# Kernel tuning notes

Hardware: AMD Instinct MI355X
Metric: run time of the kernel (lower is better)

Reference implementation:

```python
import jax, jax.numpy as jnp
import numpy as np

TOPK = 1024
C = 32
FC0 = 256
EPS_BN = 1e-5
EPS_NORM = 1e-12


def setup_inputs() -> dict:
    key = jax.random.key(0)
    ks = jax.random.split(key, 8)
    B, L = 128, 16384
    N = B * L
    x = jax.random.normal(ks[0], (N, C), dtype=jnp.float32)
    length = jnp.full((B,), L, dtype=jnp.int32)
    # conv1d_1: Conv1d(32, 1, 1) -> weight [1, 32, 1] ~ vector [32], bias [1]
    w_att = jax.random.normal(ks[1], (C,), dtype=jnp.float32) * (1.0 / np.sqrt(C))
    b_att = jnp.zeros((1,), dtype=jnp.float32)
    # bn_1: BatchNorm1d(1) (eval mode: use running stats)
    g1 = jnp.ones((1,), dtype=jnp.float32)
    be1 = jnp.zeros((1,), dtype=jnp.float32)
    rm1 = jnp.zeros((1,), dtype=jnp.float32)
    rv1 = jnp.ones((1,), dtype=jnp.float32)
    # fc_1: Linear(TOPK*C, FC0)
    fan_in = TOPK * C
    W_fc = jax.random.normal(ks[2], (FC0, fan_in), dtype=jnp.float32) * (1.0 / np.sqrt(fan_in))
    b_fc = jnp.zeros((FC0,), dtype=jnp.float32)
    # bn_2: BatchNorm1d(FC0) (eval mode)
    g2 = jnp.ones((FC0,), dtype=jnp.float32)
    be2 = jnp.zeros((FC0,), dtype=jnp.float32)
    rm2 = jnp.zeros((FC0,), dtype=jnp.float32)
    rv2 = jnp.ones((FC0,), dtype=jnp.float32)
    return {"x": x, "length": length, "w_att": w_att, "b_att": b_att,
            "g1": g1, "be1": be1, "rm1": rm1, "rv1": rv1,
            "W_fc": W_fc, "b_fc": b_fc,
            "g2": g2, "be2": be2, "rm2": rm2, "rv2": rv2}


def reference(x, length, w_att, b_att, g1, be1, rm1, rv1, W_fc, b_fc, g2, be2, rm2, rv2):
    B = length.shape[0]
    N = x.shape[0]
    L = N // B  # equal-length segments (sum(length) == N)
    # attention score: 1x1 conv over channels + BatchNorm1d(1) (eval)
    att = x @ w_att + b_att[0]                                   # [N]
    att = (att - rm1[0]) * (g1[0] / jnp.sqrt(rv1[0] + EPS_BN)) + be1[0]
    # per-segment descending sort + take top TOPK == top_k per segment
    att_b = att.reshape(B, L)                                    # [B, L]
    x_b = x.reshape(B, L, C)                                     # [B, L, C]
    _, idx = jax.lax.top_k(att_b, TOPK)                          # [B, TOPK]
    ranked = jnp.take_along_axis(x_b, idx[:, :, None], axis=1)   # [B, TOPK, C]
    flat = ranked.reshape(B, TOPK * C)                           # [B, TOPK*C]
    # fc_1 + bn_2 (eval) + L2 row-normalize
    out = flat @ W_fc.T + b_fc                                   # [B, FC0]
    out = (out - rm2) * (g2 / jnp.sqrt(rv2 + EPS_BN)) + be2
    nrm = jnp.maximum(jnp.linalg.norm(out, axis=1, keepdims=True), EPS_NORM)
    return out / nrm
```

## Files before the change

### kernel.cpp

```cpp
#include <hip/hip_runtime.h>
#include <stdint.h>

#define CC 32
#define TOPK 1024
#define FC0 256
#define HL 8192

__device__ __forceinline__ uint64_t cex(uint64_t v, int s, bool up, int t)
{
    uint64_t o = (uint64_t)__shfl_xor((unsigned long long)v, s, 64);
    bool left = ((t & s) == 0);
    uint64_t mn = v < o ? v : o;
    uint64_t mx = v < o ? o : v;
    return (left == up) ? mn : mx;
}

__global__ __launch_bounds__(256)
void k_att(const float* __restrict__ x,
           const float* __restrict__ w_att, const float* __restrict__ b_att,
           uint32_t* __restrict__ key, int N)
{
    __shared__ float tile[256][CC + 1];
    const int t = threadIdx.x;
    const size_t base = (size_t)blockIdx.x * 256;
    const float4* xv = (const float4*)(x + base * CC);
    #pragma unroll
    for (int i = 0; i < 8; ++i) {
        int e = i * 256 + t;
        float4 v = xv[e];
        int r = e >> 3, c4 = (e & 7) * 4;
        tile[r][c4 + 0] = v.x; tile[r][c4 + 1] = v.y;
        tile[r][c4 + 2] = v.z; tile[r][c4 + 3] = v.w;
    }
    __syncthreads();
    float p[8];
    #pragma unroll
    for (int j = 0; j < 8; ++j) {
        float pj = __fmul_rn(tile[t][j], w_att[j]);
        pj = __fmaf_rn(tile[t][8 + j],  w_att[8 + j],  pj);
        pj = __fmaf_rn(tile[t][16 + j], w_att[16 + j], pj);
        pj = __fmaf_rn(tile[t][24 + j], w_att[24 + j], pj);
        p[j] = pj;
    }
    float q0 = __fadd_rn(p[0], p[1]);
    float q1 = __fadd_rn(p[2], p[3]);
    float q2 = __fadd_rn(p[4], p[5]);
    float q3 = __fadd_rn(p[6], p[7]);
    float dot = __fadd_rn(__fadd_rn(q0, q1), __fadd_rn(q2, q3));
    float v = __fadd_rn(dot, b_att[0]);
    uint32_t bits = __float_as_uint(v);
    key[base + t] = (bits & 0x80000000u) ? ~bits : (bits | 0x80000000u);
}

__global__ __launch_bounds__(1024)
void k_halfsel(const uint32_t* __restrict__ key, uint64_t* __restrict__ cand)
{
    __shared__ uint32_t kv[HL];
    __shared__ uint64_t cv[2048];
    __shared__ uint32_t hist[257];
    __shared__ uint32_t s_prefix, s_k, s_cnt;
    const int t = threadIdx.x;
    const int b = blockIdx.x;
    const int lane = t & 63;
    const uint32_t halfbase = (uint32_t)(b & 1) * HL;

    {
        const uint4* ks = (const uint4*)(key + (size_t)b * HL);
        uint4 a = ks[t], c = ks[t + 1024];
        *(uint4*)&kv[t * 4] = a;
        *(uint4*)&kv[(t + 1024) * 4] = c;
    }
    if (t == 0) { s_prefix = 0; s_k = TOPK; s_cnt = 0; }
    __syncthreads();

    #pragma unroll
    for (int round = 0; round < 2; ++round) {
        if (t < 257) hist[t] = 0;
        __syncthreads();
        const uint32_t pref = s_prefix;
        const uint32_t k = s_k;
        for (int i = t; i < HL; i += 1024) {
            uint32_t u = kv[i];
            if (round == 0) atomicAdd(&hist[u >> 24], 1u);
            else if ((u >> 24) == pref) atomicAdd(&hist[(u >> 16) & 255u], 1u);
        }
        __syncthreads();
        if (t < 64) {
            int l = t;
            uint32_t h0 = hist[4*l], h1 = hist[4*l+1], h2 = hist[4*l+2], h3 = hist[4*l+3];
            uint32_t s3 = h3, s2 = h2 + s3, s1 = h1 + s2, s0 = h0 + s1;
            uint32_t tot = s0, run = tot;
            #pragma unroll
            for (int off = 1; off < 64; off <<= 1) {
                int src = l + off < 64 ? l + off : 63;
                uint32_t o = __shfl(run, src, 64);
                if (l + off < 64) run += o;
            }
            uint32_t esuf = run - tot;
            hist[4*l]   = s0 + esuf; hist[4*l+1] = s1 + esuf;
            hist[4*l+2] = s2 + esuf; hist[4*l+3] = s3 + esuf;
        }
        __syncthreads();
        if (t < 256) {
            uint32_t st = hist[t], sn = hist[t + 1];
            if (st >= k && sn < k) {
                s_prefix = (pref << 8) | (uint32_t)t;
                s_k = k - sn;
            }
        }
        __syncthreads();
    }
    const uint32_t T = s_prefix << 16;

    for (int i = t; i < HL; i += 1024) {
        bool q = kv[i] >= T;
        unsigned long long m = __ballot(q);
        uint32_t base = 0;
        if (lane == 0 && m)
            base = atomicAdd(&s_cnt, (uint32_t)__popcll(m));
        base = __shfl(base, 0);
        if (q) {
            uint32_t pos = base + (uint32_t)__popcll(m & ((1ULL << lane) - 1ULL));
            if (pos < 2048)
                cv[pos] = ((uint64_t)kv[i] << 32)
                        | (uint64_t)(uint32_t)(~(halfbase + (uint32_t)i));
        }
    }
    __syncthreads();
    const uint32_t mm = s_cnt < 2048u ? s_cnt : 2048u;
    for (int i = t; i < 2048; i += 1024)
        if ((uint32_t)i >= mm) cv[i] = 0ULL;
    __syncthreads();

    {
        uint64_t r0 = cv[t], r1 = cv[t + 1024];
        #pragma unroll
        for (int size = 2; size <= 64; size <<= 1) {
            bool up = ((t & size) == 0);
            #pragma unroll
            for (int s = size >> 1; s > 0; s >>= 1) {
                r0 = cex(r0, s, up, t);
                r1 = cex(r1, s, up, t);
            }
        }
        cv[t] = r0; cv[t + 1024] = r1;
    }
    #pragma unroll
    for (int size = 128; size <= 2048; size <<= 1) {
        for (int s = size >> 1; s >= 64; s >>= 1) {
            __syncthreads();
            int i = ((t & ~(s - 1)) << 1) | (t & (s - 1));
            int j = i | s;
            uint64_t va = cv[i], vb = cv[j];
            bool up = ((i & size) == 0);
            if (up ? (va > vb) : (va < vb)) { cv[i] = vb; cv[j] = va; }
        }
        __syncthreads();
        {
            uint64_t a0 = cv[t], a1 = cv[t + 1024];
            bool up0, up1;
            if (size <= 512)      { up0 = ((t & size) == 0); up1 = up0; }
            else if (size == 1024){ up0 = true;  up1 = false; }
            else                  { up0 = true;  up1 = true;  }
            #pragma unroll
            for (int s = 32; s > 0; s >>= 1) {
                a0 = cex(a0, s, up0, t);
                a1 = cex(a1, s, up1, t);
            }
            cv[t] = a0; cv[t + 1024] = a1;
        }
        __syncthreads();
    }
    cand[(size_t)b * TOPK + t] = cv[2047 - t];
}

__global__ __launch_bounds__(1024)
void k_merge(const uint64_t* __restrict__ cand, int* __restrict__ idx_out)
{
    __shared__ uint64_t cv[2048];
    const int t = threadIdx.x;
    const int seg = blockIdx.x;
    cv[t]        = cand[(size_t)(seg * 2) * TOPK + t];
    cv[1024 + t] = cand[(size_t)(seg * 2 + 1) * TOPK + (1023 - t)];
    __syncthreads();
    for (int s = 1024; s >= 1; s >>= 1) {
        int i = ((t & ~(s - 1)) << 1) | (t & (s - 1));
        int j = i | s;
        uint64_t va = cv[i], vb = cv[j];
        if (va < vb) { cv[i] = vb; cv[j] = va; }
        __syncthreads();
    }
    idx_out[(size_t)seg * TOPK + t] = (int)(~(uint32_t)cv[t]);
}

#define FT 64
#define KCI 32
#define NKC 128
#define KCHUNK 256

__global__ __launch_bounds__(256)
void k_fc(const float* __restrict__ x, const int* __restrict__ idx,
          const float* __restrict__ W, float* __restrict__ part, int L)
{
    __shared__ float flT[KCI][128];
    __shared__ float wT[KCI][FT];
    const int t = threadIdx.x;
    const int kc = blockIdx.x;
    const int fb = blockIdx.y * FT;
    const int tb = t >> 4, tf = t & 15;
    float acc[8][4];
    #pragma unroll
    for (int i = 0; i < 8; ++i)
        #pragma unroll
        for (int j = 0; j < 4; ++j) acc[i][j] = 0.f;

    const int b_ld = t >> 1, half = t & 1;
    for (int sub = 0; sub < KCHUNK / KCI; ++sub) {
        const int kbase = kc * KCHUNK + sub * KCI;
        const int t_idx = kbase >> 5;
        {
            int row = idx[b_ld * TOPK + t_idx];
            row = row < 0 ? 0 : (row >= L ? L - 1 : row);
            const float* src = x + ((size_t)b_ld * L + row) * CC + half * 16;
            #pragma unroll
            for (int q = 0; q < 4; ++q) {
                float4 v = ((const float4*)src)[q];
                int c0 = half * 16 + q * 4;
                flT[c0 + 0][b_ld] = v.x; flT[c0 + 1][b_ld] = v.y;
                flT[c0 + 2][b_ld] = v.z; flT[c0 + 3][b_ld] = v.w;
            }
        }
        {
            #pragma unroll
            for (int i2 = 0; i2 < 2; ++i2) {
                int e = t + i2 * 256;
                int fl = e >> 3, u = e & 7;
                const float4 v = *(const float4*)(W + (size_t)(fb + fl) * (TOPK * CC) + kbase + u * 4);
                wT[u * 4 + 0][fl] = v.x; wT[u * 4 + 1][fl] = v.y;
                wT[u * 4 + 2][fl] = v.z; wT[u * 4 + 3][fl] = v.w;
            }
        }
        __syncthreads();
        #pragma unroll
        for (int kk = 0; kk < KCI; ++kk) {
            float bb[8], ww[4];
            *(float4*)&bb[0] = *(const float4*)&flT[kk][tb * 8];
            *(float4*)&bb[4] = *(const float4*)&flT[kk][tb * 8 + 4];
            *(float4*)&ww[0] = *(const float4*)&wT[kk][tf * 4];
            #pragma unroll
            for (int i = 0; i < 8; ++i)
                #pragma unroll
                for (int j = 0; j < 4; ++j)
                    acc[i][j] = fmaf(bb[i], ww[j], acc[i][j]);
        }
        __syncthreads();
    }
    float* pbase = part + ((size_t)kc * 128) * 256 + fb + tf * 4;
    #pragma unroll
    for (int i = 0; i < 8; ++i) {
        float* dst = pbase + (size_t)(tb * 8 + i) * 256;
        ((float4*)dst)[0] = make_float4(acc[i][0], acc[i][1], acc[i][2], acc[i][3]);
    }
}

__global__ __launch_bounds__(256)
void k_post(const float* __restrict__ part, const float* __restrict__ b_fc,
            const float* __restrict__ g2, const float* __restrict__ be2,
            const float* __restrict__ rm2, const float* __restrict__ rv2,
            float* __restrict__ out)
{
    __shared__ float red[256];
    const int b = blockIdx.x, f = threadIdx.x;
    float s = 0.f;
    #pragma unroll 8
    for (int kc = 0; kc < NKC; ++kc)
        s += part[((size_t)kc * 128 + b) * 256 + f];
    s += b_fc[f];
    float o = (s - rm2[f]) * (g2[f] / sqrtf(rv2[f] + 1e-5f)) + be2[f];
    red[f] = o * o;
    __syncthreads();
    for (int st = 128; st > 0; st >>= 1) {
        if (f < st) red[f] += red[f + st];
        __syncthreads();
    }
    float nrm = fmaxf(sqrtf(red[0]), 1e-12f);
    out[(size_t)b * 256 + f] = o / nrm;
}

extern "C" void kernel_launch(void* const* d_in, const int* in_sizes, int n_in,
                              void* d_out, int out_size, void* d_ws, size_t ws_size,
                              hipStream_t stream)
{
    const float* x     = (const float*)d_in[0];
    const float* w_att = (const float*)d_in[2];
    const float* b_att = (const float*)d_in[3];
    const float* W_fc  = (const float*)d_in[8];
    const float* b_fc  = (const float*)d_in[9];
    const float* g2    = (const float*)d_in[10];
    const float* be2   = (const float*)d_in[11];
    const float* rm2   = (const float*)d_in[12];
    const float* rv2   = (const float*)d_in[13];

    const int N = in_sizes[0] / CC;
    const int B = in_sizes[1];
    const int L = N / B;

    const size_t off_key  = 0;
    const size_t off_cand = off_key + (size_t)N * 4;
    const size_t off_idx  = off_cand + (size_t)2 * B * TOPK * 8;
    const size_t off_part = off_idx + (size_t)B * TOPK * 4;

    uint8_t* ws = (uint8_t*)d_ws;
    uint32_t* key  = (uint32_t*)(ws + off_key);
    uint64_t* cand = (uint64_t*)(ws + off_cand);
    int* idx       = (int*)(ws + off_idx);
    float* part    = (float*)(ws + off_part);

    k_att<<<N / 256, 256, 0, stream>>>(x, w_att, b_att, key, N);
    k_halfsel<<<2 * B, 1024, 0, stream>>>(key, cand);
    k_merge<<<B, 1024, 0, stream>>>(cand, idx);
    dim3 g3(NKC, FC0 / FT);
    k_fc<<<g3, 256, 0, stream>>>(x, idx, W_fc, part, L);
    k_post<<<B, 256, 0, stream>>>(part, b_fc, g2, be2, rm2, rv2, (float*)d_out);
}
```

Measured before the change: 115.2 us.

## Keep half-segment keys in registers and shrink FC feature tile to 32

```diff
diff --git a/kernel.cpp b/kernel.cpp
--- a/kernel.cpp
+++ b/kernel.cpp
@@ -55,7 +55,6 @@
 __global__ __launch_bounds__(1024)
 void k_halfsel(const uint32_t* __restrict__ key, uint64_t* __restrict__ cand)
 {
-    __shared__ uint32_t kv[HL];
     __shared__ uint64_t cv[2048];
     __shared__ uint32_t hist[257];
     __shared__ uint32_t s_prefix, s_k, s_cnt;
@@ -64,11 +63,12 @@
     const int lane = t & 63;
     const uint32_t halfbase = (uint32_t)(b & 1) * HL;
 
+    uint32_t rk[8];
     {
         const uint4* ks = (const uint4*)(key + (size_t)b * HL);
         uint4 a = ks[t], c = ks[t + 1024];
-        *(uint4*)&kv[t * 4] = a;
-        *(uint4*)&kv[(t + 1024) * 4] = c;
+        rk[0] = a.x; rk[1] = a.y; rk[2] = a.z; rk[3] = a.w;
+        rk[4] = c.x; rk[5] = c.y; rk[6] = c.z; rk[7] = c.w;
     }
     if (t == 0) { s_prefix = 0; s_k = TOPK; s_cnt = 0; }
     __syncthreads();
@@ -79,8 +79,9 @@
         __syncthreads();
         const uint32_t pref = s_prefix;
         const uint32_t k = s_k;
-        for (int i = t; i < HL; i += 1024) {
-            uint32_t u = kv[i];
+        #pragma unroll
+        for (int q = 0; q < 8; ++q) {
+            uint32_t u = rk[q];
             if (round == 0) atomicAdd(&hist[u >> 24], 1u);
             else if ((u >> 24) == pref) atomicAdd(&hist[(u >> 16) & 255u], 1u);
         }
@@ -112,18 +113,20 @@
     }
     const uint32_t T = s_prefix << 16;
 
-    for (int i = t; i < HL; i += 1024) {
-        bool q = kv[i] >= T;
-        unsigned long long m = __ballot(q);
+    #pragma unroll
+    for (int q = 0; q < 8; ++q) {
+        bool qq = rk[q] >= T;
+        unsigned long long m = __ballot(qq);
         uint32_t base = 0;
         if (lane == 0 && m)
             base = atomicAdd(&s_cnt, (uint32_t)__popcll(m));
         base = __shfl(base, 0);
-        if (q) {
+        if (qq) {
+            uint32_t idx = (q < 4) ? (4u * t + q) : (HL / 2 + 4u * t + (q - 4));
             uint32_t pos = base + (uint32_t)__popcll(m & ((1ULL << lane) - 1ULL));
             if (pos < 2048)
-                cv[pos] = ((uint64_t)kv[i] << 32)
-                        | (uint64_t)(uint32_t)(~(halfbase + (uint32_t)i));
+                cv[pos] = ((uint64_t)rk[q] << 32)
+                        | (uint64_t)(uint32_t)(~(halfbase + idx));
         }
     }
     __syncthreads();
@@ -193,7 +196,7 @@
     idx_out[(size_t)seg * TOPK + t] = (int)(~(uint32_t)cv[t]);
 }
 
-#define FT 64
+#define FT 32
 #define KCI 32
 #define NKC 128
 #define KCHUNK 256
@@ -208,11 +211,11 @@
     const int kc = blockIdx.x;
     const int fb = blockIdx.y * FT;
     const int tb = t >> 4, tf = t & 15;
-    float acc[8][4];
-    #pragma unroll
-    for (int i = 0; i < 8; ++i)
-        #pragma unroll
-        for (int j = 0; j < 4; ++j) acc[i][j] = 0.f;
+    float acc[8][2];
+    #pragma unroll
+    for (int i = 0; i < 8; ++i) {
+        acc[i][0] = 0.f; acc[i][1] = 0.f;
+    }
 
     const int b_ld = t >> 1, half = t & 1;
     for (int sub = 0; sub < KCHUNK / KCI; ++sub) {
@@ -231,35 +234,31 @@
             }
         }
         {
-            #pragma unroll
-            for (int i2 = 0; i2 < 2; ++i2) {
-                int e = t + i2 * 256;
-                int fl = e >> 3, u = e & 7;
-                const float4 v = *(const float4*)(W + (size_t)(fb + fl) * (TOPK * CC) + kbase + u * 4);
-                wT[u * 4 + 0][fl] = v.x; wT[u * 4 + 1][fl] = v.y;
-                wT[u * 4 + 2][fl] = v.z; wT[u * 4 + 3][fl] = v.w;
-            }
+            int fl = t >> 3, u = t & 7;
+            const float4 v = *(const float4*)(W + (size_t)(fb + fl) * (TOPK * CC) + kbase + u * 4);
+            wT[u * 4 + 0][fl] = v.x; wT[u * 4 + 1][fl] = v.y;
+            wT[u * 4 + 2][fl] = v.z; wT[u * 4 + 3][fl] = v.w;
         }
         __syncthreads();
         #pragma unroll
         for (int kk = 0; kk < KCI; ++kk) {
-            float bb[8], ww[4];
+            float bb[8], ww[2];
             *(float4*)&bb[0] = *(const float4*)&flT[kk][tb * 8];
             *(float4*)&bb[4] = *(const float4*)&flT[kk][tb * 8 + 4];
-            *(float4*)&ww[0] = *(const float4*)&wT[kk][tf * 4];
-            #pragma unroll
-            for (int i = 0; i < 8; ++i)
-                #pragma unroll
-                for (int j = 0; j < 4; ++j)
-                    acc[i][j] = fmaf(bb[i], ww[j], acc[i][j]);
-        }
-        __syncthreads();
-    }
-    float* pbase = part + ((size_t)kc * 128) * 256 + fb + tf * 4;
+            *(float2*)&ww[0] = *(const float2*)&wT[kk][tf * 2];
+            #pragma unroll
+            for (int i = 0; i < 8; ++i) {
+                acc[i][0] = fmaf(bb[i], ww[0], acc[i][0]);
+                acc[i][1] = fmaf(bb[i], ww[1], acc[i][1]);
+            }
+        }
+        __syncthreads();
+    }
+    float* pbase = part + ((size_t)kc * 128) * 256 + fb + tf * 2;
     #pragma unroll
     for (int i = 0; i < 8; ++i) {
         float* dst = pbase + (size_t)(tb * 8 + i) * 256;
-        ((float4*)dst)[0] = make_float4(acc[i][0], acc[i][1], acc[i][2], acc[i][3]);
+        ((float2*)dst)[0] = make_float2(acc[i][0], acc[i][1]);
     }
 }
 
```

Result: slower. 122.7 us (+6.5%).

## Compute fc_1 with bf16 MFMA instead of fp32 FMA tiles

Applied to the files above, without the earlier changes.

```diff
diff --git a/kernel.cpp b/kernel.cpp
--- a/kernel.cpp
+++ b/kernel.cpp
@@ -5,6 +5,15 @@
 #define TOPK 1024
 #define FC0 256
 #define HL 8192
+
+typedef __attribute__((ext_vector_type(8))) short bf16x8;
+typedef __attribute__((ext_vector_type(4))) float f32x4;
+
+__device__ __forceinline__ ushort f2bf(float f) {
+    uint32_t u = __float_as_uint(f);
+    uint32_t r = u + 0x7FFFu + ((u >> 16) & 1u);
+    return (ushort)(r >> 16);
+}
 
 __device__ __forceinline__ uint64_t cex(uint64_t v, int s, bool up, int t)
 {
@@ -193,8 +202,6 @@
     idx_out[(size_t)seg * TOPK + t] = (int)(~(uint32_t)cv[t]);
 }
 
-#define FT 64
-#define KCI 32
 #define NKC 128
 #define KCHUNK 256
 
@@ -202,64 +209,62 @@
 void k_fc(const float* __restrict__ x, const int* __restrict__ idx,
           const float* __restrict__ W, float* __restrict__ part, int L)
 {
-    __shared__ float flT[KCI][128];
-    __shared__ float wT[KCI][FT];
+    __shared__ ushort flA[128][40];
     const int t = threadIdx.x;
+    const int w = t >> 6;
+    const int l = t & 63;
+    const int l15 = l & 15;
+    const int lq = l >> 4;
     const int kc = blockIdx.x;
-    const int fb = blockIdx.y * FT;
-    const int tb = t >> 4, tf = t & 15;
-    float acc[8][4];
-    #pragma unroll
-    for (int i = 0; i < 8; ++i)
-        #pragma unroll
-        for (int j = 0; j < 4; ++j) acc[i][j] = 0.f;
+    const int fb = blockIdx.y * 64;
+
+    f32x4 acc[8];
+    #pragma unroll
+    for (int mi = 0; mi < 8; ++mi) acc[mi] = (f32x4){0.f, 0.f, 0.f, 0.f};
 
     const int b_ld = t >> 1, half = t & 1;
-    for (int sub = 0; sub < KCHUNK / KCI; ++sub) {
-        const int kbase = kc * KCHUNK + sub * KCI;
+    const float* Wrow = W + (size_t)(fb + w * 16 + l15) * (TOPK * CC);
+
+    for (int sub = 0; sub < 8; ++sub) {
+        const int kbase = kc * KCHUNK + sub * 32;
         const int t_idx = kbase >> 5;
         {
             int row = idx[b_ld * TOPK + t_idx];
             row = row < 0 ? 0 : (row >= L ? L - 1 : row);
-            const float* src = x + ((size_t)b_ld * L + row) * CC + half * 16;
+            const float4* src = (const float4*)(x + ((size_t)b_ld * L + row) * CC + half * 16);
+            ushort* dst = &flA[b_ld][half * 16];
             #pragma unroll
             for (int q = 0; q < 4; ++q) {
-                float4 v = ((const float4*)src)[q];
-                int c0 = half * 16 + q * 4;
-                flT[c0 + 0][b_ld] = v.x; flT[c0 + 1][b_ld] = v.y;
-                flT[c0 + 2][b_ld] = v.z; flT[c0 + 3][b_ld] = v.w;
-            }
-        }
+                float4 v = src[q];
+                *(uint32_t*)(dst + q * 4)     = (uint32_t)f2bf(v.x) | ((uint32_t)f2bf(v.y) << 16);
+                *(uint32_t*)(dst + q * 4 + 2) = (uint32_t)f2bf(v.z) | ((uint32_t)f2bf(v.w) << 16);
+            }
+        }
+        bf16x8 bfrag;
         {
-            #pragma unroll
-            for (int i2 = 0; i2 < 2; ++i2) {
-                int e = t + i2 * 256;
-                int fl = e >> 3, u = e & 7;
-                const float4 v = *(const float4*)(W + (size_t)(fb + fl) * (TOPK * CC) + kbase + u * 4);
-                wT[u * 4 + 0][fl] = v.x; wT[u * 4 + 1][fl] = v.y;
-                wT[u * 4 + 2][fl] = v.z; wT[u * 4 + 3][fl] = v.w;
-            }
+            const float* wp = Wrow + kbase + lq * 8;
+            float4 w0 = ((const float4*)wp)[0];
+            float4 w1 = ((const float4*)wp)[1];
+            bfrag[0] = (short)f2bf(w0.x); bfrag[1] = (short)f2bf(w0.y);
+            bfrag[2] = (short)f2bf(w0.z); bfrag[3] = (short)f2bf(w0.w);
+            bfrag[4] = (short)f2bf(w1.x); bfrag[5] = (short)f2bf(w1.y);
+            bfrag[6] = (short)f2bf(w1.z); bfrag[7] = (short)f2bf(w1.w);
         }
         __syncthreads();
         #pragma unroll
-        for (int kk = 0; kk < KCI; ++kk) {
-            float bb[8], ww[4];
-            *(float4*)&bb[0] = *(const float4*)&flT[kk][tb * 8];
-            *(float4*)&bb[4] = *(const float4*)&flT[kk][tb * 8 + 4];
-            *(float4*)&ww[0] = *(const float4*)&wT[kk][tf * 4];
-            #pragma unroll
-            for (int i = 0; i < 8; ++i)
-                #pragma unroll
-                for (int j = 0; j < 4; ++j)
-                    acc[i][j] = fmaf(bb[i], ww[j], acc[i][j]);
-        }
-        __syncthreads();
-    }
-    float* pbase = part + ((size_t)kc * 128) * 256 + fb + tf * 4;
-    #pragma unroll
-    for (int i = 0; i < 8; ++i) {
-        float* dst = pbase + (size_t)(tb * 8 + i) * 256;
-        ((float4*)dst)[0] = make_float4(acc[i][0], acc[i][1], acc[i][2], acc[i][3]);
+        for (int mi = 0; mi < 8; ++mi) {
+            bf16x8 afrag = *(const bf16x8*)&flA[mi * 16 + l15][lq * 8];
+            acc[mi] = __builtin_amdgcn_mfma_f32_16x16x32_bf16(afrag, bfrag, acc[mi], 0, 0, 0);
+        }
+        __syncthreads();
+    }
+    float* pb = part + ((size_t)kc * 128) * 256 + fb + w * 16 + l15;
+    #pragma unroll
+    for (int mi = 0; mi < 8; ++mi) {
+        const int brow0 = mi * 16 + lq * 4;
+        #pragma unroll
+        for (int r = 0; r < 4; ++r)
+            pb[(size_t)(brow0 + r) * 256] = acc[mi][r];
     }
 }
 
@@ -319,7 +324,7 @@
     k_att<<<N / 256, 256, 0, stream>>>(x, w_att, b_att, key, N);
     k_halfsel<<<2 * B, 1024, 0, stream>>>(key, cand);
     k_merge<<<B, 1024, 0, stream>>>(cand, idx);
-    dim3 g3(NKC, FC0 / FT);
+    dim3 g3(NKC, FC0 / 64);
     k_fc<<<g3, 256, 0, stream>>>(x, idx, W_fc, part, L);
     k_post<<<B, 256, 0, stream>>>(part, b_fc, g2, be2, rm2, rv2, (float*)d_out);
 }
```

New measurement: 105.3 us (median of 2 runs). 8.6% less time.
